# Optimization experiments

Measured on AMD Instinct MI355X. Metric: run time of the kernel, lower is better.

Reference implementation:

```python
import jax, jax.numpy as jnp
import numpy as np

B, T, D = 4, 2048, 768
H = 12
DH = D // H  # 64
SCALE = DH ** -0.5


def setup_inputs() -> dict:
    key = jax.random.key(0)
    k1, k2, k3, k4 = jax.random.split(key, 4)
    x = jax.random.normal(k1, (B, T, D), dtype=jnp.float32)
    # torch nn.Linear weights: stored [out, in], applied as x @ W.T
    Wqkv = jax.random.normal(k2, (3 * D, D), dtype=jnp.float32) * (D ** -0.5)
    Wproj = jax.random.normal(k3, (D, D), dtype=jnp.float32) * (D ** -0.5)
    bproj = jax.random.normal(k4, (D,), dtype=jnp.float32) * 0.01
    return {"x": x, "Wqkv": Wqkv, "Wproj": Wproj, "bproj": bproj}


def reference(x, Wqkv, Wproj, bproj):
    Bb, Tt, C = x.shape
    qkv = x @ Wqkv.T                       # [B,T,3D]
    q, k, v = jnp.split(qkv, 3, axis=-1)   # each [B,T,D]
    q = q.reshape(Bb, Tt, H, DH)
    k = k.reshape(Bb, Tt, H, DH)
    v = v.reshape(Bb, Tt, H, DH)
    # scores [B,H,T,T]
    att = jnp.einsum('bqhd,bkhd->bhqk', q, k) * SCALE
    causal = jnp.triu(jnp.ones((Tt, Tt), dtype=bool), k=1)
    att = jnp.where(causal, -jnp.inf, att)
    att = jax.nn.softmax(att, axis=-1)
    out = jnp.einsum('bhqk,bkhd->bqhd', att, v).reshape(Bb, Tt, C)
    return out @ Wproj.T + bproj
```

## Files before the change

kernel.cpp:

```cpp
#include <hip/hip_runtime.h>
#include <hip/hip_bf16.h>


#define BATCH  4
#define SEQ    2048
#define DMODEL 768
#define NH     12
#define DHEAD  64
static constexpr float SCALE_LOG2E = 0.125f * 1.4426950408889634f;

#define N_X  (8192 * 768)
#define N_WQ (2304 * 768)
#define N_WP (768 * 768)

typedef __bf16 v8bf __attribute__((ext_vector_type(8)));
typedef float  v4f  __attribute__((ext_vector_type(4)));

__device__ __forceinline__ v8bf cvt8(const float* __restrict__ p) {
    const float4 a = ((const float4*)p)[0];
    const float4 b = ((const float4*)p)[1];
    v8bf r;
    r[0] = (__bf16)a.x; r[1] = (__bf16)a.y; r[2] = (__bf16)a.z; r[3] = (__bf16)a.w;
    r[4] = (__bf16)b.x; r[5] = (__bf16)b.y; r[6] = (__bf16)b.z; r[7] = (__bf16)b.w;
    return r;
}

__device__ __forceinline__ void async_copy16(__bf16* lds, const __bf16* g) {
    __builtin_amdgcn_global_load_lds(
        (const __attribute__((address_space(1))) void*)g,
        (__attribute__((address_space(3))) void*)lds, 16, 0, 0);
}

__global__ __launch_bounds__(256) void cvt_kernel(
        const float* __restrict__ x, const float* __restrict__ Wq,
        const float* __restrict__ Wp, __bf16* __restrict__ xb,
        __bf16* __restrict__ Wqb, __bf16* __restrict__ Wpb) {
    const long e = ((long)blockIdx.x * 256 + threadIdx.x) * 8;
    const float* src;
    __bf16* dst;
    if (e < N_X)             { src = x  + e;               dst = xb  + e; }
    else if (e < N_X + N_WQ) { src = Wq + (e - N_X);        dst = Wqb + (e - N_X); }
    else                     { src = Wp + (e - N_X - N_WQ); dst = Wpb + (e - N_X - N_WQ); }
    *(v8bf*)dst = cvt8(src);
}

__global__ __launch_bounds__(256) void qkv_gemm(
        const __bf16* __restrict__ xb, const __bf16* __restrict__ Wb,
        __bf16* __restrict__ Qb, __bf16* __restrict__ Kb, __bf16* __restrict__ Vtb) {
    __shared__ __bf16 As[2][128 * 32], Bs[2][128 * 32];
    const int lane = threadIdx.x & 63, wave = threadIdx.x >> 6;
    const int nb = blockIdx.x % 18, mb = blockIdx.x / 18;
    const int r16 = lane & 15, quad = lane >> 4;
    const int wm = (wave >> 1) * 64, wn = (wave & 1) * 64;
    const __bf16* Asrc = xb + (size_t)mb * 128 * DMODEL;
    const __bf16* Bsrc = Wb + (size_t)nb * 128 * DMODEL;

    const int srow = wave * 16 + (lane >> 2);
    const int sg   = lane & 3;
    const int g    = sg ^ ((srow >> 1) & 3);
    const size_t soff0 = (size_t)srow * DMODEL + g * 8;
    const size_t soff1 = (size_t)(srow + 64) * DMODEL + g * 8;
    const int ld0 = wave * 512;
    const int ld1 = 2048 + wave * 512;
    const int p_rd = quad ^ ((r16 >> 1) & 3);

    async_copy16(&As[0][ld0], Asrc + soff0);
    async_copy16(&As[0][ld1], Asrc + soff1);
    async_copy16(&Bs[0][ld0], Bsrc + soff0);
    async_copy16(&Bs[0][ld1], Bsrc + soff1);

    v4f acc[4][4] = {};
    for (int c = 0; c < 24; ++c) {
        const int cur = c & 1;
        __syncthreads();
        v8bf a[4], b[4];
#pragma unroll
        for (int i = 0; i < 4; ++i)
            a[i] = *(const v8bf*)&As[cur][(wm + 16 * i + r16) * 32 + p_rd * 8];
#pragma unroll
        for (int j = 0; j < 4; ++j)
            b[j] = *(const v8bf*)&Bs[cur][(wn + 16 * j + r16) * 32 + p_rd * 8];
        if (c + 1 < 24) {
            const int nxt = cur ^ 1;
            const size_t k1 = (c + 1) * 32;
            async_copy16(&As[nxt][ld0], Asrc + soff0 + k1);
            async_copy16(&As[nxt][ld1], Asrc + soff1 + k1);
            async_copy16(&Bs[nxt][ld0], Bsrc + soff0 + k1);
            async_copy16(&Bs[nxt][ld1], Bsrc + soff1 + k1);
        }
#pragma unroll
        for (int i = 0; i < 4; ++i)
#pragma unroll
            for (int j = 0; j < 4; ++j)
                acc[i][j] = __builtin_amdgcn_mfma_f32_16x16x32_bf16(
                    a[i], b[j], acc[i][j], 0, 0, 0);
    }

    const int seg = nb / 6;
    const int nl0 = (nb % 6) * 128 + wn;
#pragma unroll
    for (int j = 0; j < 4; ++j) {
        const int n = nl0 + 16 * j + r16;
        const int h = n >> 6, d = n & 63;
#pragma unroll
        for (int i = 0; i < 4; ++i) {
            const int mrow = mb * 128 + wm + 16 * i + quad * 4;
#pragma unroll
            for (int r = 0; r < 4; ++r) {
                const int m = mrow + r;
                const int bidx = m >> 11, t = m & (SEQ - 1);
                const size_t base = ((size_t)(bidx * NH + h)) * SEQ * DHEAD;
                if (seg == 0)
                    Qb[base + (size_t)t * DHEAD + d] = (__bf16)(acc[i][j][r] * SCALE_LOG2E);
                else if (seg == 1)
                    Kb[base + (size_t)t * DHEAD + d] = (__bf16)acc[i][j][r];
                else
                    Vtb[base + (size_t)d * SEQ + t] = (__bf16)acc[i][j][r];
            }
        }
    }
}

__global__ __launch_bounds__(256, 3) void attn_kernel(
        const __bf16* __restrict__ Qb, const __bf16* __restrict__ Kb,
        const __bf16* __restrict__ Vtb, __bf16* __restrict__ attnb) {
    __shared__ __bf16 Ks[2][64 * 32];
    __shared__ __bf16 Vs[2][64 * 32];
    __shared__ __align__(16) __bf16 Pl[4][32 * 72];
    const int lane = threadIdx.x & 63;
    const int wave = threadIdx.x >> 6;
    const int bh = blockIdx.x % 48;
    const int qt = 15 - (blockIdx.x / 48);
    const int q0 = qt * 128 + wave * 32;
    const int r16 = lane & 15, quad = lane >> 4;

    const __bf16* Q  = Qb  + (size_t)bh * SEQ * DHEAD;
    const __bf16* K  = Kb  + (size_t)bh * SEQ * DHEAD;
    const __bf16* Vt = Vtb + (size_t)bh * DHEAD * SEQ;

    const int srow  = wave * 16 + (lane >> 2);
    const int skoff = (lane & 3) * 8;
    __bf16* kd0 = &Ks[0][wave * 512];
    __bf16* kd1 = &Ks[1][wave * 512];
    __bf16* vd0 = &Vs[0][wave * 512];
    __bf16* vd1 = &Vs[1][wave * 512];

    v8bf aq[2][2];
#pragma unroll
    for (int i = 0; i < 2; ++i)
#pragma unroll
        for (int kk = 0; kk < 2; ++kk)
            aq[i][kk] = *(const v8bf*)(Q + (size_t)(q0 + 16 * i + r16) * DHEAD
                                         + kk * 32 + quad * 8);

    v8bf vones;
#pragma unroll
    for (int j = 0; j < 8; ++j) vones[j] = (__bf16)1.0f;

    v4f oacc[2][4] = {};
    v4f lacc[2] = {};

    const int nchunks = 2 * (qt + 1);
    async_copy16(kd0, K + (size_t)srow * DHEAD + skoff);
    async_copy16(kd1, K + (size_t)srow * DHEAD + 32 + skoff);
    async_copy16(vd0, Vt + (size_t)srow * SEQ + skoff);
    async_copy16(vd1, Vt + (size_t)srow * SEQ + 32 + skoff);

    for (int c = 0; c < nchunks; ++c) {
        const int k0 = c * 64;
        __syncthreads();
        v8bf bk[4][2], bv[2][4];
#pragma unroll
        for (int s = 0; s < 4; ++s)
#pragma unroll
            for (int kk = 0; kk < 2; ++kk)
                bk[s][kk] = *(const v8bf*)&Ks[kk][(16 * s + r16) * 32 + quad * 8];
#pragma unroll
        for (int kk = 0; kk < 2; ++kk)
#pragma unroll
            for (int n = 0; n < 4; ++n)
                bv[kk][n] = *(const v8bf*)&Vs[kk][(16 * n + r16) * 32 + quad * 8];
        __syncthreads();
        if (c + 1 < nchunks) {
            const int k1 = k0 + 64;
            async_copy16(kd0, K + (size_t)(k1 + srow) * DHEAD + skoff);
            async_copy16(kd1, K + (size_t)(k1 + srow) * DHEAD + 32 + skoff);
            async_copy16(vd0, Vt + (size_t)srow * SEQ + k1 + skoff);
            async_copy16(vd1, Vt + (size_t)srow * SEQ + k1 + 32 + skoff);
        }
        if (k0 > q0 + 31) continue;

        v4f sc[2][4] = {};
#pragma unroll
        for (int kk = 0; kk < 2; ++kk)
#pragma unroll
            for (int i = 0; i < 2; ++i)
#pragma unroll
                for (int s = 0; s < 4; ++s)
                    sc[i][s] = __builtin_amdgcn_mfma_f32_16x16x32_bf16(
                        aq[i][kk], bk[s][kk], sc[i][s], 0, 0, 0);

        if (k0 + 63 > q0) {
#pragma unroll
            for (int i = 0; i < 2; ++i)
#pragma unroll
                for (int s = 0; s < 4; ++s)
#pragma unroll
                    for (int r = 0; r < 4; ++r) {
                        const int row = q0 + 16 * i + quad * 4 + r;
                        const int col = k0 + 16 * s + r16;
                        if (col > row) sc[i][s][r] = -1e30f;
                    }
        }

#pragma unroll
        for (int i = 0; i < 2; ++i)
#pragma unroll
            for (int s = 0; s < 4; ++s)
#pragma unroll
                for (int r = 0; r < 4; ++r)
                    sc[i][s][r] = __builtin_exp2f(sc[i][s][r] - 32.0f);

#pragma unroll
        for (int i = 0; i < 2; ++i)
#pragma unroll
            for (int s = 0; s < 4; ++s)
#pragma unroll
                for (int r = 0; r < 4; ++r)
                    Pl[wave][(16 * i + quad * 4 + r) * 72 + 16 * s + r16] =
                        (__bf16)sc[i][s][r];
        __builtin_amdgcn_s_waitcnt(0);

        v8bf ap[2][2];
#pragma unroll
        for (int i = 0; i < 2; ++i)
#pragma unroll
            for (int kk = 0; kk < 2; ++kk)
                ap[i][kk] = *(const v8bf*)&Pl[wave][(16 * i + r16) * 72 + kk * 32 + quad * 8];
#pragma unroll
        for (int kk = 0; kk < 2; ++kk)
#pragma unroll
            for (int i = 0; i < 2; ++i) {
#pragma unroll
                for (int n = 0; n < 4; ++n)
                    oacc[i][n] = __builtin_amdgcn_mfma_f32_16x16x32_bf16(
                        ap[i][kk], bv[kk][n], oacc[i][n], 0, 0, 0);
                lacc[i] = __builtin_amdgcn_mfma_f32_16x16x32_bf16(
                    ap[i][kk], vones, lacc[i], 0, 0, 0);
            }
    }

    const int b = bh / NH, h = bh - b * NH;
#pragma unroll
    for (int i = 0; i < 2; ++i)
#pragma unroll
        for (int r = 0; r < 4; ++r) {
            const float inv = 1.0f / lacc[i][r];
            const int t = q0 + 16 * i + quad * 4 + r;
#pragma unroll
            for (int n = 0; n < 4; ++n) {
                const int d = 16 * n + r16;
                attnb[((size_t)(b * SEQ + t)) * DMODEL + h * DHEAD + d] =
                    (__bf16)(oacc[i][n][r] * inv);
            }
        }
}

__global__ __launch_bounds__(256) void proj_gemm(
        const __bf16* __restrict__ Ab, const __bf16* __restrict__ Wb,
        const float* __restrict__ bias, float* __restrict__ out) {
    __shared__ __bf16 As[2][128 * 32], Bs[2][128 * 32];
    const int lane = threadIdx.x & 63, wave = threadIdx.x >> 6;
    const int nb = blockIdx.x % 6, mb = blockIdx.x / 6;
    const int r16 = lane & 15, quad = lane >> 4;
    const int wm = (wave >> 1) * 64, wn = (wave & 1) * 64;
    const __bf16* Asrc = Ab + (size_t)mb * 128 * DMODEL;
    const __bf16* Bsrc = Wb + (size_t)nb * 128 * DMODEL;

    const int srow = wave * 16 + (lane >> 2);
    const int sg   = lane & 3;
    const int g    = sg ^ ((srow >> 1) & 3);
    const size_t soff0 = (size_t)srow * DMODEL + g * 8;
    const size_t soff1 = (size_t)(srow + 64) * DMODEL + g * 8;
    const int ld0 = wave * 512;
    const int ld1 = 2048 + wave * 512;
    const int p_rd = quad ^ ((r16 >> 1) & 3);

    async_copy16(&As[0][ld0], Asrc + soff0);
    async_copy16(&As[0][ld1], Asrc + soff1);
    async_copy16(&Bs[0][ld0], Bsrc + soff0);
    async_copy16(&Bs[0][ld1], Bsrc + soff1);

    v4f acc[4][4] = {};
    for (int c = 0; c < 24; ++c) {
        const int cur = c & 1;
        __syncthreads();
        v8bf a[4], b[4];
#pragma unroll
        for (int i = 0; i < 4; ++i)
            a[i] = *(const v8bf*)&As[cur][(wm + 16 * i + r16) * 32 + p_rd * 8];
#pragma unroll
        for (int j = 0; j < 4; ++j)
            b[j] = *(const v8bf*)&Bs[cur][(wn + 16 * j + r16) * 32 + p_rd * 8];
        if (c + 1 < 24) {
            const int nxt = cur ^ 1;
            const size_t k1 = (c + 1) * 32;
            async_copy16(&As[nxt][ld0], Asrc + soff0 + k1);
            async_copy16(&As[nxt][ld1], Asrc + soff1 + k1);
            async_copy16(&Bs[nxt][ld0], Bsrc + soff0 + k1);
            async_copy16(&Bs[nxt][ld1], Bsrc + soff1 + k1);
        }
#pragma unroll
        for (int i = 0; i < 4; ++i)
#pragma unroll
            for (int j = 0; j < 4; ++j)
                acc[i][j] = __builtin_amdgcn_mfma_f32_16x16x32_bf16(
                    a[i], b[j], acc[i][j], 0, 0, 0);
    }

#pragma unroll
    for (int j = 0; j < 4; ++j) {
        const int n = nb * 128 + wn + 16 * j + r16;
        const float bv = bias[n];
#pragma unroll
        for (int i = 0; i < 4; ++i) {
            const int mrow = mb * 128 + wm + 16 * i + quad * 4;
#pragma unroll
            for (int r = 0; r < 4; ++r)
                out[(size_t)(mrow + r) * DMODEL + n] = acc[i][j][r] + bv;
        }
    }
}

extern "C" void kernel_launch(void* const* d_in, const int* in_sizes, int n_in,
                              void* d_out, int out_size, void* d_ws, size_t ws_size,
                              hipStream_t stream) {
    const float* x     = (const float*)d_in[0];
    const float* Wqkv  = (const float*)d_in[1];
    const float* Wproj = (const float*)d_in[2];
    const float* bproj = (const float*)d_in[3];
    float* out = (float*)d_out;

    char* ws = (char*)d_ws;
    const size_t tsz = (size_t)BATCH * NH * SEQ * DHEAD * sizeof(__bf16);
    __bf16* Qb    = (__bf16*)(ws);
    __bf16* Kb    = (__bf16*)(ws + tsz);
    __bf16* Vtb   = (__bf16*)(ws + 2 * tsz);
    __bf16* xb    = (__bf16*)(ws + 3 * tsz);
    __bf16* attnb = (__bf16*)(ws + 3 * tsz);
    __bf16* Wqb   = (__bf16*)(ws + 4 * tsz);
    __bf16* Wpb   = (__bf16*)(ws + 4 * tsz + (size_t)N_WQ * 2);

    cvt_kernel<<<dim3((N_X + N_WQ + N_WP) / (8 * 256)), dim3(256), 0, stream>>>(
        x, Wqkv, Wproj, xb, Wqb, Wpb);
    qkv_gemm<<<dim3(64 * 18), dim3(256), 0, stream>>>(xb, Wqb, Qb, Kb, Vtb);
    attn_kernel<<<dim3(16 * 48), dim3(256), 0, stream>>>(Qb, Kb, Vtb, attnb);
    proj_gemm<<<dim3(64 * 6), dim3(256), 0, stream>>>(attnb, Wpb, bproj, out);
}
```

Measured before the change: 233.4 us.

## Double-buffer K/V tiles in attention, swizzle LDS, and halve proj GEMM M-tile

The attention kernel now keeps two K/V LDS buffers, so the next chunk's async copy no longer has to wait behind a second __syncthreads per iteration. The K/V tiles also use an XOR swizzle on the 8-element groups to reduce LDS bank conflicts on fragment reads. Separately, the projection GEMM shrinks its M-tile from 128 to 64 rows and doubles the grid, aiming for better CU occupancy and load balance on a small GEMM. The costs are doubled attention LDS, which may lower blocks per CU, and more redundant weight loads in the projection.

```diff
diff --git a/kernel.cpp b/kernel.cpp
--- a/kernel.cpp
+++ b/kernel.cpp
@@ -124,8 +124,8 @@
 __global__ __launch_bounds__(256, 3) void attn_kernel(
         const __bf16* __restrict__ Qb, const __bf16* __restrict__ Kb,
         const __bf16* __restrict__ Vtb, __bf16* __restrict__ attnb) {
-    __shared__ __bf16 Ks[2][64 * 32];
-    __shared__ __bf16 Vs[2][64 * 32];
+    __shared__ __bf16 Ks[2][2][64 * 32];
+    __shared__ __bf16 Vs[2][2][64 * 32];
     __shared__ __align__(16) __bf16 Pl[4][32 * 72];
     const int lane = threadIdx.x & 63;
     const int wave = threadIdx.x >> 6;
@@ -138,12 +138,11 @@
     const __bf16* K  = Kb  + (size_t)bh * SEQ * DHEAD;
     const __bf16* Vt = Vtb + (size_t)bh * DHEAD * SEQ;
 
-    const int srow  = wave * 16 + (lane >> 2);
-    const int skoff = (lane & 3) * 8;
-    __bf16* kd0 = &Ks[0][wave * 512];
-    __bf16* kd1 = &Ks[1][wave * 512];
-    __bf16* vd0 = &Vs[0][wave * 512];
-    __bf16* vd1 = &Vs[1][wave * 512];
+    const int srow = wave * 16 + (lane >> 2);
+    const int sg   = lane & 3;
+    const int g    = sg ^ ((srow >> 1) & 3);
+    const int ldw  = wave * 512;
+    const int p_rd = quad ^ ((r16 >> 1) & 3);
 
     v8bf aq[2][2];
 #pragma unroll
@@ -161,32 +160,37 @@
     v4f lacc[2] = {};
 
     const int nchunks = 2 * (qt + 1);
-    async_copy16(kd0, K + (size_t)srow * DHEAD + skoff);
-    async_copy16(kd1, K + (size_t)srow * DHEAD + 32 + skoff);
-    async_copy16(vd0, Vt + (size_t)srow * SEQ + skoff);
-    async_copy16(vd1, Vt + (size_t)srow * SEQ + 32 + skoff);
+#pragma unroll
+    for (int kk = 0; kk < 2; ++kk) {
+        async_copy16(&Ks[0][kk][ldw], K + (size_t)srow * DHEAD + kk * 32 + g * 8);
+        async_copy16(&Vs[0][kk][ldw], Vt + (size_t)srow * SEQ + kk * 32 + g * 8);
+    }
 
     for (int c = 0; c < nchunks; ++c) {
         const int k0 = c * 64;
+        const int cur = c & 1;
         __syncthreads();
         v8bf bk[4][2], bv[2][4];
 #pragma unroll
         for (int s = 0; s < 4; ++s)
 #pragma unroll
             for (int kk = 0; kk < 2; ++kk)
-                bk[s][kk] = *(const v8bf*)&Ks[kk][(16 * s + r16) * 32 + quad * 8];
+                bk[s][kk] = *(const v8bf*)&Ks[cur][kk][(16 * s + r16) * 32 + p_rd * 8];
 #pragma unroll
         for (int kk = 0; kk < 2; ++kk)
 #pragma unroll
             for (int n = 0; n < 4; ++n)
-                bv[kk][n] = *(const v8bf*)&Vs[kk][(16 * n + r16) * 32 + quad * 8];
-        __syncthreads();
+                bv[kk][n] = *(const v8bf*)&Vs[cur][kk][(16 * n + r16) * 32 + p_rd * 8];
         if (c + 1 < nchunks) {
+            const int nxt = cur ^ 1;
             const int k1 = k0 + 64;
-            async_copy16(kd0, K + (size_t)(k1 + srow) * DHEAD + skoff);
-            async_copy16(kd1, K + (size_t)(k1 + srow) * DHEAD + 32 + skoff);
-            async_copy16(vd0, Vt + (size_t)srow * SEQ + k1 + skoff);
-            async_copy16(vd1, Vt + (size_t)srow * SEQ + k1 + 32 + skoff);
+#pragma unroll
+            for (int kk = 0; kk < 2; ++kk) {
+                async_copy16(&Ks[nxt][kk][ldw],
+                             K + (size_t)(k1 + srow) * DHEAD + kk * 32 + g * 8);
+                async_copy16(&Vs[nxt][kk][ldw],
+                             Vt + (size_t)srow * SEQ + k1 + kk * 32 + g * 8);
+            }
         }
         if (k0 > q0 + 31) continue;
 
@@ -269,35 +273,35 @@
 __global__ __launch_bounds__(256) void proj_gemm(
         const __bf16* __restrict__ Ab, const __bf16* __restrict__ Wb,
         const float* __restrict__ bias, float* __restrict__ out) {
-    __shared__ __bf16 As[2][128 * 32], Bs[2][128 * 32];
+    __shared__ __bf16 As[2][64 * 32], Bs[2][128 * 32];
     const int lane = threadIdx.x & 63, wave = threadIdx.x >> 6;
     const int nb = blockIdx.x % 6, mb = blockIdx.x / 6;
     const int r16 = lane & 15, quad = lane >> 4;
-    const int wm = (wave >> 1) * 64, wn = (wave & 1) * 64;
-    const __bf16* Asrc = Ab + (size_t)mb * 128 * DMODEL;
+    const int wm = (wave >> 1) * 32, wn = (wave & 1) * 64;
+    const __bf16* Asrc = Ab + (size_t)mb * 64 * DMODEL;
     const __bf16* Bsrc = Wb + (size_t)nb * 128 * DMODEL;
 
     const int srow = wave * 16 + (lane >> 2);
     const int sg   = lane & 3;
     const int g    = sg ^ ((srow >> 1) & 3);
-    const size_t soff0 = (size_t)srow * DMODEL + g * 8;
-    const size_t soff1 = (size_t)(srow + 64) * DMODEL + g * 8;
+    const size_t soffA  = (size_t)srow * DMODEL + g * 8;
+    const size_t soffB0 = soffA;
+    const size_t soffB1 = (size_t)(srow + 64) * DMODEL + g * 8;
     const int ld0 = wave * 512;
     const int ld1 = 2048 + wave * 512;
     const int p_rd = quad ^ ((r16 >> 1) & 3);
 
-    async_copy16(&As[0][ld0], Asrc + soff0);
-    async_copy16(&As[0][ld1], Asrc + soff1);
-    async_copy16(&Bs[0][ld0], Bsrc + soff0);
-    async_copy16(&Bs[0][ld1], Bsrc + soff1);
-
-    v4f acc[4][4] = {};
+    async_copy16(&As[0][ld0], Asrc + soffA);
+    async_copy16(&Bs[0][ld0], Bsrc + soffB0);
+    async_copy16(&Bs[0][ld1], Bsrc + soffB1);
+
+    v4f acc[2][4] = {};
     for (int c = 0; c < 24; ++c) {
         const int cur = c & 1;
         __syncthreads();
-        v8bf a[4], b[4];
-#pragma unroll
-        for (int i = 0; i < 4; ++i)
+        v8bf a[2], b[4];
+#pragma unroll
+        for (int i = 0; i < 2; ++i)
             a[i] = *(const v8bf*)&As[cur][(wm + 16 * i + r16) * 32 + p_rd * 8];
 #pragma unroll
         for (int j = 0; j < 4; ++j)
@@ -305,13 +309,12 @@
         if (c + 1 < 24) {
             const int nxt = cur ^ 1;
             const size_t k1 = (c + 1) * 32;
-            async_copy16(&As[nxt][ld0], Asrc + soff0 + k1);
-            async_copy16(&As[nxt][ld1], Asrc + soff1 + k1);
-            async_copy16(&Bs[nxt][ld0], Bsrc + soff0 + k1);
-            async_copy16(&Bs[nxt][ld1], Bsrc + soff1 + k1);
-        }
-#pragma unroll
-        for (int i = 0; i < 4; ++i)
+            async_copy16(&As[nxt][ld0], Asrc + soffA + k1);
+            async_copy16(&Bs[nxt][ld0], Bsrc + soffB0 + k1);
+            async_copy16(&Bs[nxt][ld1], Bsrc + soffB1 + k1);
+        }
+#pragma unroll
+        for (int i = 0; i < 2; ++i)
 #pragma unroll
             for (int j = 0; j < 4; ++j)
                 acc[i][j] = __builtin_amdgcn_mfma_f32_16x16x32_bf16(
@@ -323,8 +326,8 @@
         const int n = nb * 128 + wn + 16 * j + r16;
         const float bv = bias[n];
 #pragma unroll
-        for (int i = 0; i < 4; ++i) {
-            const int mrow = mb * 128 + wm + 16 * i + quad * 4;
+        for (int i = 0; i < 2; ++i) {
+            const int mrow = mb * 64 + wm + 16 * i + quad * 4;
 #pragma unroll
             for (int r = 0; r < 4; ++r)
                 out[(size_t)(mrow + r) * DMODEL + n] = acc[i][j][r] + bv;
@@ -355,5 +358,5 @@
         x, Wqkv, Wproj, xb, Wqb, Wpb);
     qkv_gemm<<<dim3(64 * 18), dim3(256), 0, stream>>>(xb, Wqb, Qb, Kb, Vtb);
     attn_kernel<<<dim3(16 * 48), dim3(256), 0, stream>>>(Qb, Kb, Vtb, attnb);
-    proj_gemm<<<dim3(64 * 6), dim3(256), 0, stream>>>(attnb, Wpb, bproj, out);
-}
+    proj_gemm<<<dim3(128 * 6), dim3(256), 0, stream>>>(attnb, Wpb, bproj, out);
+}
```

After: 233.0 us. About the same (-0.2%).
